# Kernel tuning notes

Hardware: AMD Instinct MI355X
Metric: run time of the kernel (lower is better)

The kernel has to match this reference:

```python
import jax, jax.numpy as jnp
import numpy as np

B, L, E, H = 2, 2048, 1024, 16
D = E // H  # head_dim = 64


def setup_inputs() -> dict:
    key = jax.random.key(0)
    ks = jax.random.split(key, 9)
    s = 1.0 / np.sqrt(E)
    return {
        "query": jax.random.normal(ks[0], (B, L, E), jnp.float32),
        "key": jax.random.normal(ks[1], (B, L, E), jnp.float32),
        "value": jax.random.normal(ks[2], (B, L, E), jnp.float32),
        # torch Linear weights are [out_features, in_features]
        "Wq": jax.random.uniform(ks[3], (E, E), jnp.float32, -s, s),
        "bq": jnp.zeros((E,), jnp.float32),
        "Wk": jax.random.uniform(ks[4], (E, E), jnp.float32, -s, s),  # k_proj, no bias (add_bias_kv=False)
        "Wv": jax.random.uniform(ks[5], (E, E), jnp.float32, -s, s),  # v_proj, no bias
        "Wo": jax.random.uniform(ks[6], (E, E), jnp.float32, -s, s),
        "bo": jnp.zeros((E,), jnp.float32),
    }


def reference(query, key, value, Wq, bq, Wk, Wv, Wo, bo):
    # Projections (torch Linear: y = x @ W.T + b)
    q = query @ Wq.T + bq          # [B, L, E]
    k = key @ Wk.T                 # [B, L, E]
    v = value @ Wv.T               # [B, L, E]
    # Split heads
    q = q.reshape(B, L, H, D)
    k = k.reshape(B, L, H, D)
    v = v.reshape(B, L, H, D)
    # Scaled dot-product attention; the source's chunked online-softmax
    # computes exactly softmax(q k^T / sqrt(D)) v.
    q = q / jnp.sqrt(jnp.asarray(D, q.dtype))
    scores = jnp.einsum("bqhd,bkhd->bhqk", q, k)      # [B, H, L, L]
    probs = jax.nn.softmax(scores, axis=-1)
    out = jnp.einsum("bhqk,bkhd->bqhd", probs, v)     # [B, L, H, D]
    out = out.reshape(B, L, E)
    return out @ Wo.T + bo
```

## Files before the change

kernel.cpp:

```cpp
#include <hip/hip_runtime.h>

typedef __bf16 bf16;
typedef __bf16 bf16x8 __attribute__((ext_vector_type(8)));
typedef __bf16 bf16x4 __attribute__((ext_vector_type(4)));
typedef float  f32x4  __attribute__((ext_vector_type(4)));

#define MFMA_BF16(a, b, c) __builtin_amdgcn_mfma_f32_16x16x32_bf16((a), (b), (c), 0, 0, 0)


__device__ __forceinline__ void async_load16(const bf16* g, const bf16* l) {
    auto gp = (const __attribute__((address_space(1))) unsigned int*)(unsigned long long)(const void*)g;
    auto lp = (__attribute__((address_space(3))) unsigned int*)(unsigned int)(unsigned long long)(const void*)l;
    __builtin_amdgcn_global_load_lds(gp, lp, 16, 0, 0);
}

__global__ void cvt_bf16_kernel(
    const float* __restrict__ s0, const float* __restrict__ s1, const float* __restrict__ s2,
    const float* __restrict__ s3, const float* __restrict__ s4, const float* __restrict__ s5,
    const float* __restrict__ s6,
    bf16* __restrict__ d0, bf16* __restrict__ d1, bf16* __restrict__ d2,
    bf16* __restrict__ d3, bf16* __restrict__ d4, bf16* __restrict__ d5,
    bf16* __restrict__ d6)
{
    unsigned e = (blockIdx.x * 256 + threadIdx.x) * 4;
    const float* src; bf16* dst; unsigned off;
    if (e < 12582912u) {
        unsigned which = e >> 22;
        src = which == 0 ? s0 : (which == 1 ? s1 : s2);
        dst = which == 0 ? d0 : (which == 1 ? d1 : d2);
        off = e & 4194303u;
    } else {
        unsigned ew = e - 12582912u;
        unsigned which = ew >> 20;
        src = which == 0 ? s3 : (which == 1 ? s4 : (which == 2 ? s5 : s6));
        dst = which == 0 ? d3 : (which == 1 ? d4 : (which == 2 ? d5 : d6));
        off = ew & 1048575u;
    }
    float4 f = *(const float4*)(src + off);
    bf16x4 o;
    o.x = (bf16)f.x; o.y = (bf16)f.y; o.z = (bf16)f.z; o.w = (bf16)f.w;
    *(bf16x4*)(dst + off) = o;
}

template<int BN>
__global__ __launch_bounds__(256, (BN == 128) ? 2 : 4) void gemm4_kernel(
    const bf16* __restrict__ Xq, const bf16* __restrict__ Xk, const bf16* __restrict__ Xv,
    const bf16* __restrict__ Ao,
    const bf16* __restrict__ Wq, const bf16* __restrict__ Wk, const bf16* __restrict__ Wv,
    const bf16* __restrict__ Wo,
    const float* __restrict__ bq, const float* __restrict__ bo,
    bf16* __restrict__ Qs, bf16* __restrict__ Ksw, bf16* __restrict__ Vsw,
    float* __restrict__ out, int zbase)
{
    const int z = zbase + blockIdx.z;
    const bf16 *Amat, *Bmat;
    if (z == 0)      { Amat = Wq; Bmat = Xq; }
    else if (z == 1) { Amat = Wk; Bmat = Xk; }
    else if (z == 2) { Amat = Xv; Bmat = Wv; }
    else             { Amat = Wo; Bmat = Ao; }

    const int m0 = (z == 2 ? blockIdx.y : blockIdx.x) * 128;
    const int n0 = (z == 2 ? blockIdx.x : blockIdx.y) * BN;

    __shared__ __align__(16) bf16 lA[128 * 32];
    __shared__ __align__(16) bf16 lB[BN * 32];

    const int tid  = threadIdx.x;
    const int w    = tid >> 6;
    const int lane = tid & 63;
    const int lm   = lane & 15;
    const int g    = lane >> 4;
    const int wm   = (w & 1) * 64;
    const int wn   = (w >> 1) * (BN / 2);
    constexpr int NT = BN / 32;
    constexpr int T  = (128 + BN) / 64;

    f32x4 acc[4][NT] = {};

    for (int kb = 0; kb < 32; kb++) {
        __syncthreads();
#pragma unroll
        for (int t = 0; t < T; t++) {
            int s   = (t * 4 + w) * 64 + lane;
            int row = s >> 2;
            int gs  = s & 3;
            int gg  = gs ^ ((row >> 1) & 3);
            if (row < 128)
                async_load16(Amat + (size_t)(m0 + row) * 1024 + kb * 32 + gg * 8, lA + s * 8);
            else
                async_load16(Bmat + (size_t)(n0 + row - 128) * 1024 + kb * 32 + gg * 8,
                             lB + (s - 512) * 8);
        }
        __syncthreads();

        bf16x8 af[4], bfr[NT];
#pragma unroll
        for (int mt = 0; mt < 4; mt++) {
            int row = wm + mt * 16 + lm;
            af[mt] = *(const bf16x8*)(lA + row * 32 + ((g ^ ((row >> 1) & 3)) << 3));
        }
#pragma unroll
        for (int nt = 0; nt < NT; nt++) {
            int row = wn + nt * 16 + lm;
            bfr[nt] = *(const bf16x8*)(lB + row * 32 + ((g ^ ((row >> 1) & 3)) << 3));
        }
#pragma unroll
        for (int mt = 0; mt < 4; mt++)
#pragma unroll
            for (int nt = 0; nt < NT; nt++)
                acc[mt][nt] = MFMA_BF16(af[mt], bfr[nt], acc[mt][nt]);
    }

    if (z == 3) {
#pragma unroll
        for (int mt = 0; mt < 4; mt++) {
            int mb = m0 + wm + mt * 16 + g * 4;
            f32x4 bov = *(const f32x4*)(bo + mb);
#pragma unroll
            for (int nt = 0; nt < NT; nt++) {
                int n = n0 + wn + nt * 16 + lm;
                f32x4 val;
#pragma unroll
                for (int r = 0; r < 4; r++) val[r] = acc[mt][nt][r] + bov[r];
                *(f32x4*)(out + (size_t)n * 1024 + mb) = val;
            }
        }
    } else if (z == 2) {
#pragma unroll
        for (int mt = 0; mt < 4; mt++) {
            int mb   = m0 + wm + mt * 16 + g * 4;
            int b    = mb >> 11;
            int lpos = mb & 2047;
            int kb2  = lpos >> 6, kc = (lpos >> 5) & 1, gv = (lpos >> 3) & 3, j0 = lpos & 7;
#pragma unroll
            for (int nt = 0; nt < NT; nt++) {
                int n = n0 + wn + nt * 16 + lm;
                int h = n >> 6, mt2 = (n >> 4) & 3, lmv = n & 15;
                bf16x4 ov;
#pragma unroll
                for (int r = 0; r < 4; r++) ov[r] = (bf16)acc[mt][nt][r];
                *(bf16x4*)(Vsw + (size_t)(b * 16 + h) * 131072 +
                           (size_t)((kb2 * 8 + mt2 * 2 + kc) * 64 + gv * 16 + lmv) * 8 + j0) = ov;
            }
        }
    } else if (z == 1) {
#pragma unroll
        for (int mt = 0; mt < 4; mt++) {
            int mb = m0 + wm + mt * 16 + g * 4;
            int h  = mb >> 6;
            int f  = (mb >> 5) & 1, gk = (mb >> 3) & 3, j0 = mb & 7;
#pragma unroll
            for (int nt = 0; nt < NT; nt++) {
                int n    = n0 + wn + nt * 16 + lm;
                int b    = n >> 11;
                int lpos = n & 2047;
                int kb2  = lpos >> 6;
                int rem  = lpos & 63;
                int c    = ((rem >> 4) & 2) | ((rem >> 2) & 1);
                int lmk  = ((rem >> 1) & 12) | (rem & 3);
                bf16x4 ov;
#pragma unroll
                for (int r = 0; r < 4; r++) ov[r] = (bf16)acc[mt][nt][r];
                *(bf16x4*)(Ksw + (size_t)(b * 16 + h) * 131072 +
                           (size_t)((kb2 * 8 + c * 2 + f) * 64 + gk * 16 + lmk) * 8 + j0) = ov;
            }
        }
    } else {
        const float qscale = 0.18033688011112042f;
#pragma unroll
        for (int mt = 0; mt < 4; mt++) {
            int mb  = m0 + wm + mt * 16 + g * 4;
            int h   = mb >> 6;
            int dd0 = mb & 63;
            f32x4 bqv = *(const f32x4*)(bq + mb);
#pragma unroll
            for (int nt = 0; nt < NT; nt++) {
                int n    = n0 + wn + nt * 16 + lm;
                int b    = n >> 11;
                int lpos = n & 2047;
                bf16x4 ov;
#pragma unroll
                for (int r = 0; r < 4; r++)
                    ov[r] = (bf16)((acc[mt][nt][r] + bqv[r]) * qscale);
                *(bf16x4*)(Qs + (size_t)((b * 16 + h) * 2048 + lpos) * 64 + dd0) = ov;
            }
        }
    }
}

__global__ __launch_bounds__(256, 2) void attn_kernel(
    const bf16* __restrict__ Qs, const bf16* __restrict__ Ksw,
    const bf16* __restrict__ Vsw, bf16* __restrict__ attn)
{
    const int tid  = threadIdx.x;
    const int w    = tid >> 6;
    const int lane = tid & 63;
    const int lm   = lane & 15;
    const int g    = lane >> 4;
    const int i    = blockIdx.x;
    const int bh   = ((i & 7) << 2) | ((i >> 3) & 3);
    const int q0   = (i >> 5) * 128 + w * 32;

    const bf16* Qh = Qs  + (size_t)bh * 131072;
    const bf16* Kh = Ksw + (size_t)bh * 131072;
    const bf16* Vh = Vsw + (size_t)bh * 131072;

    __shared__ __align__(16) bf16 ost[4][32 * 72];

    bf16x8 qf[2][2];
#pragma unroll
    for (int qi = 0; qi < 2; qi++)
#pragma unroll
        for (int f = 0; f < 2; f++)
            qf[qi][f] = *(const bf16x8*)(Qh + (size_t)(q0 + qi * 16 + lm) * 64 + f * 32 + g * 8);

    const f32x4 fzero = {0.0f, 0.0f, 0.0f, 0.0f};
    f32x4 o[2][4] = {};
    float lsum[2] = {0.0f, 0.0f};

    bf16x8 kf[8], vf[8];
#pragma unroll
    for (int t = 0; t < 8; t++)
        kf[t] = *(const bf16x8*)(Kh + ((size_t)t * 64 + lane) * 8);
#pragma unroll
    for (int t = 0; t < 8; t++)
        vf[t] = *(const bf16x8*)(Vh + ((size_t)t * 64 + lane) * 8);

    for (int kb = 0; kb < 32; kb++) {
        const int kn = (kb < 31) ? kb + 1 : 31;
        const bf16* Kn = Kh + (size_t)kn * 4096;
        const bf16* Vn = Vh + (size_t)kn * 4096;

        f32x4 s[2][4];
        __builtin_amdgcn_s_setprio(1);
#pragma unroll
        for (int c = 0; c < 4; c++) {
            s[0][c] = MFMA_BF16(kf[2 * c],     qf[0][0], fzero);
            s[1][c] = MFMA_BF16(kf[2 * c],     qf[1][0], fzero);
            s[0][c] = MFMA_BF16(kf[2 * c + 1], qf[0][1], s[0][c]);
            s[1][c] = MFMA_BF16(kf[2 * c + 1], qf[1][1], s[1][c]);
        }
        __builtin_amdgcn_s_setprio(0);

#pragma unroll
        for (int t = 0; t < 8; t++)
            kf[t] = *(const bf16x8*)(Kn + ((size_t)t * 64 + lane) * 8);

        bf16x8 pb[2][2];
#pragma unroll
        for (int qi = 0; qi < 2; qi++) {
            float part = 0.0f;
#pragma unroll
            for (int kc = 0; kc < 2; kc++)
#pragma unroll
                for (int r = 0; r < 4; r++) {
                    float p0 = __builtin_amdgcn_exp2f(s[qi][2 * kc][r]);
                    float p1 = __builtin_amdgcn_exp2f(s[qi][2 * kc + 1][r]);
                    pb[qi][kc][r]     = (bf16)p0;
                    pb[qi][kc][r + 4] = (bf16)p1;
                    part += p0 + p1;
                }
            lsum[qi] += part;
        }

        __builtin_amdgcn_s_setprio(1);
#pragma unroll
        for (int kc = 0; kc < 2; kc++)
#pragma unroll
            for (int mt = 0; mt < 4; mt++) {
                o[0][mt] = MFMA_BF16(vf[mt * 2 + kc], pb[0][kc], o[0][mt]);
                o[1][mt] = MFMA_BF16(vf[mt * 2 + kc], pb[1][kc], o[1][mt]);
            }
        __builtin_amdgcn_s_setprio(0);

#pragma unroll
        for (int t = 0; t < 8; t++)
            vf[t] = *(const bf16x8*)(Vn + ((size_t)t * 64 + lane) * 8);
    }

#pragma unroll
    for (int qi = 0; qi < 2; qi++) {
        lsum[qi] += __shfl_xor(lsum[qi], 16);
        lsum[qi] += __shfl_xor(lsum[qi], 32);
    }

    const int b = bh >> 4, h = bh & 15;
#pragma unroll
    for (int qi = 0; qi < 2; qi++) {
        float inv = 1.0f / lsum[qi];
#pragma unroll
        for (int mt = 0; mt < 4; mt++) {
            bf16x4 ov;
#pragma unroll
            for (int r = 0; r < 4; r++) ov[r] = (bf16)(o[qi][mt][r] * inv);
            *(bf16x4*)(ost[w] + (qi * 16 + lm) * 72 + mt * 16 + g * 4) = ov;
        }
    }
#pragma unroll
    for (int it = 0; it < 4; it++) {
        int cc = it * 64 + lane;
        int q  = cc >> 3, ch = cc & 7;
        bf16x8 t = *(const bf16x8*)(ost[w] + q * 72 + ch * 8);
        *(bf16x8*)(attn + (size_t)(b * 2048 + q0 + q) * 1024 + h * 64 + ch * 8) = t;
    }
}

extern "C" void kernel_launch(void* const* d_in, const int* in_sizes, int n_in,
                              void* d_out, int out_size, void* d_ws, size_t ws_size,
                              hipStream_t stream) {
    const float* query = (const float*)d_in[0];
    const float* key   = (const float*)d_in[1];
    const float* value = (const float*)d_in[2];
    const float* Wq    = (const float*)d_in[3];
    const float* bq    = (const float*)d_in[4];
    const float* Wk    = (const float*)d_in[5];
    const float* Wv    = (const float*)d_in[6];
    const float* Wo    = (const float*)d_in[7];
    const float* bo    = (const float*)d_in[8];

    char* ws = (char*)d_ws;
    bf16* Xq  = (bf16*)(ws);
    bf16* Xk  = (bf16*)(ws + ((size_t)8  << 20));
    bf16* Xv  = (bf16*)(ws + ((size_t)16 << 20));
    bf16* Wqb = (bf16*)(ws + ((size_t)24 << 20));
    bf16* Wkb = (bf16*)(ws + ((size_t)26 << 20));
    bf16* Wvb = (bf16*)(ws + ((size_t)28 << 20));
    bf16* Wob = (bf16*)(ws + ((size_t)30 << 20));
    bf16* Qs  = (bf16*)(ws + ((size_t)32 << 20));
    bf16* Ksw = (bf16*)(ws + ((size_t)40 << 20));
    bf16* Vsw = (bf16*)(ws + ((size_t)48 << 20));
    bf16* attn = Xq;

    cvt_bf16_kernel<<<dim3(16384, 1, 1), 256, 0, stream>>>(
        query, key, value, Wq, Wk, Wv, Wo, Xq, Xk, Xv, Wqb, Wkb, Wvb, Wob);

    gemm4_kernel<128><<<dim3(8, 32, 3), 256, 0, stream>>>(
        Xq, Xk, Xv, attn, Wqb, Wkb, Wvb, Wob, bq, bo, Qs, Ksw, Vsw, (float*)d_out, 0);

    attn_kernel<<<dim3(512, 1, 1), 256, 0, stream>>>(Qs, Ksw, Vsw, attn);

    gemm4_kernel<64><<<dim3(8, 64, 1), 256, 0, stream>>>(
        Xq, Xk, Xv, attn, Wqb, Wkb, Wvb, Wob, bq, bo, Qs, Ksw, Vsw, (float*)d_out, 3);
}
```

Before: 214.6 us.

## Load two K-slices per barrier and remap block indices for L2 locality

The GEMM main loop now loads two 32-wide K slices into separate LDS buffers before each barrier pair, halving the number of synchronisations and giving more MFMA work per sync. Block indices are also remapped so that consecutive workgroups (likely spread across XCDs in groups of 8) share tiles and get better L2 reuse. The cost is doubled LDS usage, which may reduce occupancy, and the remap assumes gridDim.x is 8 and gridDim.y is a multiple of 8.

Result: faster. 206.3 us (-3.9%).

```diff
diff --git a/kernel.cpp b/kernel.cpp
--- a/kernel.cpp
+++ b/kernel.cpp
@@ -59,11 +59,17 @@
     else if (z == 2) { Amat = Xv; Bmat = Wv; }
     else             { Amat = Wo; Bmat = Ao; }
 
-    const int m0 = (z == 2 ? blockIdx.y : blockIdx.x) * 128;
-    const int n0 = (z == 2 ? blockIdx.x : blockIdx.y) * BN;
-
-    __shared__ __align__(16) bf16 lA[128 * 32];
-    __shared__ __align__(16) bf16 lB[BN * 32];
+    const int flat = blockIdx.x + 8 * blockIdx.y;
+    const int c    = flat & 7;
+    const int j    = flat >> 3;
+    const int ft   = j & 7;
+    const int tt   = c * (gridDim.y >> 3) + (j >> 3);
+
+    const int m0 = (z == 2 ? tt : ft) * 128;
+    const int n0 = (z == 2 ? ft : tt) * BN;
+
+    __shared__ __align__(16) bf16 lA[2][128 * 32];
+    __shared__ __align__(16) bf16 lB[2][BN * 32];
 
     const int tid  = threadIdx.x;
     const int w    = tid >> 6;
@@ -77,38 +83,46 @@
 
     f32x4 acc[4][NT] = {};
 
-    for (int kb = 0; kb < 32; kb++) {
+    for (int kb2 = 0; kb2 < 16; kb2++) {
         __syncthreads();
 #pragma unroll
-        for (int t = 0; t < T; t++) {
-            int s   = (t * 4 + w) * 64 + lane;
-            int row = s >> 2;
-            int gs  = s & 3;
-            int gg  = gs ^ ((row >> 1) & 3);
-            if (row < 128)
-                async_load16(Amat + (size_t)(m0 + row) * 1024 + kb * 32 + gg * 8, lA + s * 8);
-            else
-                async_load16(Bmat + (size_t)(n0 + row - 128) * 1024 + kb * 32 + gg * 8,
-                             lB + (s - 512) * 8);
+        for (int st = 0; st < 2; st++) {
+            int kb = kb2 * 2 + st;
+#pragma unroll
+            for (int t = 0; t < T; t++) {
+                int s   = (t * 4 + w) * 64 + lane;
+                int row = s >> 2;
+                int gs  = s & 3;
+                int gg  = gs ^ ((row >> 1) & 3);
+                if (row < 128)
+                    async_load16(Amat + (size_t)(m0 + row) * 1024 + kb * 32 + gg * 8,
+                                 lA[st] + s * 8);
+                else
+                    async_load16(Bmat + (size_t)(n0 + row - 128) * 1024 + kb * 32 + gg * 8,
+                                 lB[st] + (s - 512) * 8);
+            }
         }
         __syncthreads();
 
-        bf16x8 af[4], bfr[NT];
-#pragma unroll
-        for (int mt = 0; mt < 4; mt++) {
-            int row = wm + mt * 16 + lm;
-            af[mt] = *(const bf16x8*)(lA + row * 32 + ((g ^ ((row >> 1) & 3)) << 3));
-        }
-#pragma unroll
-        for (int nt = 0; nt < NT; nt++) {
-            int row = wn + nt * 16 + lm;
-            bfr[nt] = *(const bf16x8*)(lB + row * 32 + ((g ^ ((row >> 1) & 3)) << 3));
-        }
-#pragma unroll
-        for (int mt = 0; mt < 4; mt++)
-#pragma unroll
-            for (int nt = 0; nt < NT; nt++)
-                acc[mt][nt] = MFMA_BF16(af[mt], bfr[nt], acc[mt][nt]);
+#pragma unroll
+        for (int st = 0; st < 2; st++) {
+            bf16x8 af[4], bfr[NT];
+#pragma unroll
+            for (int mt = 0; mt < 4; mt++) {
+                int row = wm + mt * 16 + lm;
+                af[mt] = *(const bf16x8*)(lA[st] + row * 32 + ((g ^ ((row >> 1) & 3)) << 3));
+            }
+#pragma unroll
+            for (int nt = 0; nt < NT; nt++) {
+                int row = wn + nt * 16 + lm;
+                bfr[nt] = *(const bf16x8*)(lB[st] + row * 32 + ((g ^ ((row >> 1) & 3)) << 3));
+            }
+#pragma unroll
+            for (int mt = 0; mt < 4; mt++)
+#pragma unroll
+                for (int nt = 0; nt < NT; nt++)
+                    acc[mt][nt] = MFMA_BF16(af[mt], bfr[nt], acc[mt][nt]);
+        }
     }
 
     if (z == 3) {
@@ -156,13 +170,13 @@
                 int lpos = n & 2047;
                 int kb2  = lpos >> 6;
                 int rem  = lpos & 63;
-                int c    = ((rem >> 4) & 2) | ((rem >> 2) & 1);
+                int cc   = ((rem >> 4) & 2) | ((rem >> 2) & 1);
                 int lmk  = ((rem >> 1) & 12) | (rem & 3);
                 bf16x4 ov;
 #pragma unroll
                 for (int r = 0; r < 4; r++) ov[r] = (bf16)acc[mt][nt][r];
                 *(bf16x4*)(Ksw + (size_t)(b * 16 + h) * 131072 +
-                           (size_t)((kb2 * 8 + c * 2 + f) * 64 + gk * 16 + lmk) * 8 + j0) = ov;
+                           (size_t)((kb2 * 8 + cc * 2 + f) * 64 + gk * 16 + lmk) * 8 + j0) = ov;
             }
         }
     } else {
```
